# Performance work log

Hardware: AMD Instinct MI355X
Metric: run time of the kernel (lower is better)

The kernel has to match this reference:

```python
import jax, jax.numpy as jnp
import numpy as np
from jax import lax

BN_EPS = 1e-5
PAD = ((2, 3), (1, 2))  # 'same' padding for kernel (6,4): H pad 5 -> (2,3), W pad 3 -> (1,2)
DN = ('NCHW', 'OIHW', 'NCHW')


def _conv_block(x, w, b, g, bt, m, v, pool):
    # pool(bn(relu(conv(pad(x))))) as in the torch module (eval-mode BN)
    x = lax.conv_general_dilated(x, w, (1, 1), PAD, dimension_numbers=DN)
    x = jax.nn.relu(x + b[None, :, None, None])
    scale = g / jnp.sqrt(v + BN_EPS)
    x = (x - m[None, :, None, None]) * scale[None, :, None, None] + bt[None, :, None, None]
    win = (1, 1) + pool
    return lax.reduce_window(x, -jnp.inf, lax.max, win, win, 'VALID')


def _fc_bn(x, w, b, g, bt, m, v):
    x = jax.nn.relu(x @ w.T + b)
    return (x - m) * (g / jnp.sqrt(v + BN_EPS)) + bt


def _apply_cnn(x, p):
    x = x[:, None, :, :]  # [N,1,72,64]
    x = _conv_block(x, p['conv1_w'], p['conv1_b'], p['bnc1_g'], p['bnc1_b'], p['bnc1_m'], p['bnc1_v'], (2, 2))
    x = _conv_block(x, p['conv2_w'], p['conv2_b'], p['bnc2_g'], p['bnc2_b'], p['bnc2_m'], p['bnc2_v'], (2, 2))
    x = _conv_block(x, p['conv3_w'], p['conv3_b'], p['bnc3_g'], p['bnc3_b'], p['bnc3_m'], p['bnc3_v'], (3, 4))
    x = x.reshape(x.shape[0], 6 * 4 * 64)  # NCHW contiguous flatten matches torch .view
    x = _fc_bn(x, p['fc1_w'], p['fc1_b'], p['bnf1_g'], p['bnf1_b'], p['bnf1_m'], p['bnf1_v'])
    x = _fc_bn(x, p['fc2_w'], p['fc2_b'], p['bnf2_g'], p['bnf2_b'], p['bnf2_m'], p['bnf2_v'])
    x = _fc_bn(x, p['fc3_w'], p['fc3_b'], p['bnf3_g'], p['bnf3_b'], p['bnf3_m'], p['bnf3_v'])
    # F.normalize(x, p=2, dim=1) with eps=1e-12
    nrm = jnp.linalg.norm(x, axis=1, keepdims=True)
    return x / jnp.maximum(nrm, 1e-12)


def _ssm(embeds):
    # pairwise L2 distances via Gram trick (replaces the O(n^2) python loop)
    sq = jnp.sum(embeds * embeds, axis=1)  # [n]
    d2 = sq[:, None] + sq[None, :] - 2.0 * (embeds @ embeds.T)
    dist = jnp.sqrt(jnp.maximum(d2, 1e-12))
    dist = jnp.where(d2 > 0, dist, 0.0)  # exact zeros on diagonal, nan-safe grad
    return dist / jnp.max(dist)


def setup_inputs() -> dict:
    key = jax.random.key(0)
    ks = iter(jax.random.split(key, 64))
    d = {'x': jax.random.normal(next(ks), (512, 72, 64), jnp.float32)}

    def nrm(shape, s=0.05):
        return jax.random.normal(next(ks), shape, jnp.float32) * s

    def add_bn(name, c):
        d[name + '_g'] = 1.0 + nrm((c,))
        d[name + '_b'] = nrm((c,))
        d[name + '_m'] = nrm((c,), 0.1)
        d[name + '_v'] = 0.5 + jax.random.uniform(next(ks), (c,), jnp.float32)

    d['conv1_w'] = nrm((16, 1, 6, 4), 0.2);  d['conv1_b'] = nrm((16,));  add_bn('bnc1', 16)
    d['conv2_w'] = nrm((32, 16, 6, 4), 0.1); d['conv2_b'] = nrm((32,));  add_bn('bnc2', 32)
    d['conv3_w'] = nrm((64, 32, 6, 4), 0.05); d['conv3_b'] = nrm((64,)); add_bn('bnc3', 64)
    d['fc1_w'] = nrm((512, 1536), 0.03); d['fc1_b'] = nrm((512,)); add_bn('bnf1', 512)
    d['fc2_w'] = nrm((256, 512), 0.05);  d['fc2_b'] = nrm((256,)); add_bn('bnf2', 256)
    d['fc3_w'] = nrm((128, 256), 0.07);  d['fc3_b'] = nrm((128,)); add_bn('bnf3', 128)
    return d


def reference(x,
              conv1_w, conv1_b, bnc1_g, bnc1_b, bnc1_m, bnc1_v,
              conv2_w, conv2_b, bnc2_g, bnc2_b, bnc2_m, bnc2_v,
              conv3_w, conv3_b, bnc3_g, bnc3_b, bnc3_m, bnc3_v,
              fc1_w, fc1_b, bnf1_g, bnf1_b, bnf1_m, bnf1_v,
              fc2_w, fc2_b, bnf2_g, bnf2_b, bnf2_m, bnf2_v,
              fc3_w, fc3_b, bnf3_g, bnf3_b, bnf3_m, bnf3_v):
    p = dict(conv1_w=conv1_w, conv1_b=conv1_b, bnc1_g=bnc1_g, bnc1_b=bnc1_b, bnc1_m=bnc1_m, bnc1_v=bnc1_v,
             conv2_w=conv2_w, conv2_b=conv2_b, bnc2_g=bnc2_g, bnc2_b=bnc2_b, bnc2_m=bnc2_m, bnc2_v=bnc2_v,
             conv3_w=conv3_w, conv3_b=conv3_b, bnc3_g=bnc3_g, bnc3_b=bnc3_b, bnc3_m=bnc3_m, bnc3_v=bnc3_v,
             fc1_w=fc1_w, fc1_b=fc1_b, bnf1_g=bnf1_g, bnf1_b=bnf1_b, bnf1_m=bnf1_m, bnf1_v=bnf1_v,
             fc2_w=fc2_w, fc2_b=fc2_b, bnf2_g=bnf2_g, bnf2_b=bnf2_b, bnf2_m=bnf2_m, bnf2_v=bnf2_v,
             fc3_w=fc3_w, fc3_b=fc3_b, bnf3_g=bnf3_g, bnf3_b=bnf3_b, bnf3_m=bnf3_m, bnf3_v=bnf3_v)
    embeds = _apply_cnn(x, p)  # [n, 128], L2-normalized
    return _ssm(embeds)        # [n, n]
```

## Files before the change

kernel.cpp:

```cpp
#include <hip/hip_runtime.h>
#include <math.h>


#define BN_EPS 1e-5f

typedef __attribute__((ext_vector_type(8))) short short8;
typedef __attribute__((ext_vector_type(4))) float f32x4;

__device__ __forceinline__ unsigned short f2bf(float f) {
    unsigned u = __float_as_uint(f);
    u += 0x7fffu + ((u >> 16) & 1u);
    return (unsigned short)(u >> 16);
}

__global__ __launch_bounds__(256) void repack_k(
    const float* __restrict__ w1, const float* __restrict__ w2,
    const float* __restrict__ w3,
    const float* __restrict__ fw1, const float* __restrict__ fw2,
    const float* __restrict__ fw3,
    unsigned short* __restrict__ wT1b,
    unsigned short* __restrict__ wT2b, unsigned short* __restrict__ wT3b,
    unsigned short* __restrict__ fw1b, unsigned short* __restrict__ fw2b,
    unsigned short* __restrict__ fw3b, unsigned* __restrict__ mxslot)
{
    int t = blockIdx.x * 256 + threadIdx.x;
    if (t == 0) *mxslot = 0u;
    if (t < 512) {
        int k = t & 31, oc = t >> 5;
        wT1b[t] = (k < 24) ? f2bf(w1[oc * 24 + k]) : (unsigned short)0;
    }
    if (t < 12288) {
        int k = t & 31, oc = (t >> 5) & 31, kk = t >> 10;
        int ky = kk >> 1, kxp = kk & 1;
        int hi = k >> 4, ic = k & 15;
        int kx = 2 * kxp + hi;
        wT2b[t] = f2bf(w2[((oc * 16 + ic) * 6 + ky) * 4 + kx]);
    }
    if (t < 49152) {
        int ic = t & 31, oc = (t >> 5) & 63, kk = t >> 11;
        int ky = kk >> 2, kx = kk & 3;
        wT3b[t] = f2bf(w3[((oc * 32 + ic) * 6 + ky) * 4 + kx]);
    }
    if (t < 786432) fw1b[t] = f2bf(fw1[t]);
    if (t < 131072) fw2b[t] = f2bf(fw2[t]);
    if (t < 32768)  fw3b[t] = f2bf(fw3[t]);
}

__global__ __launch_bounds__(512) void conv_all(
    const float* __restrict__ x, const unsigned short* __restrict__ wT1,
    const unsigned short* __restrict__ wT2, const unsigned short* __restrict__ wT3,
    const float* __restrict__ c1b, const float* __restrict__ g1,
    const float* __restrict__ b1, const float* __restrict__ m1,
    const float* __restrict__ v1,
    const float* __restrict__ c2b, const float* __restrict__ g2,
    const float* __restrict__ b2, const float* __restrict__ m2,
    const float* __restrict__ v2,
    const float* __restrict__ c3b, const float* __restrict__ g3,
    const float* __restrict__ b3, const float* __restrict__ m3,
    const float* __restrict__ v3,
    unsigned short* __restrict__ out3)
{
    __shared__ __align__(16) unsigned short s_out1[41 * 36 * 16];
    __shared__ __align__(16) unsigned short s_un[24 * 20 * 32];
    const int tid = threadIdx.x, nl = blockIdx.x;
    const int lane = tid & 63, wave = tid >> 6;
    const int n = lane & 15, q = lane >> 4;
    unsigned short* pa = s_un;
    unsigned short* pb = s_un + 5372;

    {
        unsigned* z32 = (unsigned*)s_un;
        for (int i = tid; i < 5372; i += 512) z32[i] = 0u;
        uint4 z4; z4.x = z4.y = z4.z = z4.w = 0u;
        for (int pc = tid; pc < 324; pc += 512) {
            int row, colc;
            if (pc < 180) { row = pc / 36; colc = pc % 36; if (row >= 2) row += 36; }
            else { int pz = pc - 180; row = 2 + (pz >> 2); colc = (pz & 3) ? 32 + (pz & 3) : 0; }
            uint4* d = (uint4*)(s_out1 + ((size_t)row * 36 + colc) * 16);
            d[0] = z4; d[1] = z4;
        }
    }
    __syncthreads();
    {
        const float4* src = (const float4*)(x + (size_t)nl * 4608);
        for (int i = tid; i < 1152; i += 512) {
            float4 val = src[i];
            int f = i * 4, row = (f >> 6) + 2, c = (f & 63) + 1;
            unsigned short h0 = f2bf(val.x), h1 = f2bf(val.y);
            unsigned short h2 = f2bf(val.z), h3 = f2bf(val.w);
            unsigned short* ap = pa + row * 68 + c;
            ap[0] = h0; ap[1] = h1; ap[2] = h2; ap[3] = h3;
            unsigned* bp = (unsigned*)(pb + row * 68 + c + 1);
            bp[0] = (unsigned)h0 | ((unsigned)h1 << 16);
            bp[1] = (unsigned)h2 | ((unsigned)h3 << 16);
        }
    }
    const float sc1 = g1[n] * rsqrtf(v1[n] + BN_EPS);
    const float bb1 = c1b[n];
    const float mm1 = b1[n] - m1[n] * sc1;
    const short8 bfr1 = *(const short8*)(wT1 + n * 32 + q * 8);
    __syncthreads();

    for (int i = 0; i < 36; ++i) {
        int t = wave * 36 + i;
        int pooled = 4 * t + (n >> 2);
        int ph = pooled >> 5, pw = pooled & 31;
        int py = (n >> 1) & 1, px = n & 1;
        int oh = 2 * ph + py, ow = 2 * pw + px;
        int r0 = (oh + 2 * q) * 68;
        const unsigned* base = px ? (const unsigned*)(pb + r0 + ow + 1)
                                  : (const unsigned*)(pa + r0 + ow);
        uint4 uu;
        uu.x = base[0];  uu.y = base[1];
        uu.z = base[34]; uu.w = base[35];
        short8 afr = *reinterpret_cast<short8*>(&uu);
        f32x4 acc = (f32x4){0.f, 0.f, 0.f, 0.f};
        acc = __builtin_amdgcn_mfma_f32_16x16x32_bf16(afr, bfr1, acc, 0, 0, 0);
        int po = 4 * t + q, oph = po >> 5, opw = po & 31;
        float mx = fmaxf(fmaxf(acc[0], acc[1]), fmaxf(acc[2], acc[3]));
        float val = fmaxf(mx + bb1, 0.f) * sc1 + mm1;
        s_out1[((oph + 2) * 36 + (opw + 1)) * 16 + n] = f2bf(val);
    }
    __syncthreads();
    {
        uint4 z4; z4.x = z4.y = z4.z = z4.w = 0u;
        for (int pc = tid; pc < 192; pc += 512) {
            int row, colc;
            if (pc < 120) { row = pc / 20; colc = pc % 20; if (row >= 2) row += 18; }
            else { int pz = pc - 120; row = 2 + (pz >> 2); colc = (pz & 3) ? 16 + (pz & 3) : 0; }
            uint4* d = (uint4*)(s_un + ((size_t)row * 20 + colc) * 32);
            d[0] = z4; d[1] = z4; d[2] = z4; d[3] = z4;
        }
    }
    float bnb2[2], bns2[2], bnm2[2];
#pragma unroll
    for (int nt = 0; nt < 2; ++nt) {
        int oc = nt * 16 + n;
        float sc = g2[oc] * rsqrtf(v2[oc] + BN_EPS);
        bnb2[nt] = c2b[oc]; bns2[nt] = sc; bnm2[nt] = b2[oc] - m2[oc] * sc;
    }
    __syncthreads();

    for (int pp = wave; pp < 36; pp += 8) {
        int ph = pp >> 1, half = pp & 1;
        f32x4 acc[2][2];
#pragma unroll
        for (int ab = 0; ab < 2; ++ab)
#pragma unroll
            for (int nt = 0; nt < 2; ++nt) acc[ab][nt] = (f32x4){0.f, 0.f, 0.f, 0.f};
#pragma unroll
        for (int ky = 0; ky < 6; ++ky)
#pragma unroll
            for (int kxp = 0; kxp < 2; ++kxp) {
                int kk = ky * 2 + kxp;
                short8 w0 = *(const short8*)(wT2 + ((size_t)(kk * 32 + n) * 32) + q * 8);
                short8 w1 = *(const short8*)(wT2 + ((size_t)(kk * 32 + 16 + n) * 32) + q * 8);
                int col = half * 16 + n + 2 * kxp;
#pragma unroll
                for (int ab = 0; ab < 2; ++ab) {
                    int row = 2 * ph + ab + ky;
                    short8 afr = *(const short8*)(s_out1 + ((size_t)(row * 36 + col) * 16) + q * 8);
                    acc[ab][0] = __builtin_amdgcn_mfma_f32_16x16x32_bf16(afr, w0, acc[ab][0], 0, 0, 0);
                    acc[ab][1] = __builtin_amdgcn_mfma_f32_16x16x32_bf16(afr, w1, acc[ab][1], 0, 0, 0);
                }
            }
        int pw0 = half * 8 + q * 2;
#pragma unroll
        for (int nt = 0; nt < 2; ++nt) {
            int oc = nt * 16 + n;
            float p0 = fmaxf(fmaxf(acc[0][nt][0], acc[0][nt][1]),
                             fmaxf(acc[1][nt][0], acc[1][nt][1]));
            float p1 = fmaxf(fmaxf(acc[0][nt][2], acc[0][nt][3]),
                             fmaxf(acc[1][nt][2], acc[1][nt][3]));
            p0 = fmaxf(p0 + bnb2[nt], 0.f) * bns2[nt] + bnm2[nt];
            p1 = fmaxf(p1 + bnb2[nt], 0.f) * bns2[nt] + bnm2[nt];
            s_un[((size_t)(ph + 2) * 20 + (pw0 + 1)) * 32 + oc] = f2bf(p0);
            s_un[((size_t)(ph + 2) * 20 + (pw0 + 2)) * 32 + oc] = f2bf(p1);
        }
    }
    __syncthreads();

    for (int ch = wave; ch < 12; ch += 8) {
        int pr = ch >> 1, nth = ch & 1;
        f32x4 acc[3][2];
#pragma unroll
        for (int r = 0; r < 3; ++r)
#pragma unroll
            for (int t2 = 0; t2 < 2; ++t2) acc[r][t2] = (f32x4){0.f, 0.f, 0.f, 0.f};
#pragma unroll
        for (int ky = 0; ky < 6; ++ky)
#pragma unroll
            for (int kx = 0; kx < 4; ++kx) {
                int kk = ky * 4 + kx;
                short8 w0 = *(const short8*)(wT3 + ((size_t)(kk * 64 + nth * 32 + n) * 32) + q * 8);
                short8 w1 = *(const short8*)(wT3 + ((size_t)(kk * 64 + nth * 32 + 16 + n) * 32) + q * 8);
#pragma unroll
                for (int r = 0; r < 3; ++r) {
                    int row = 3 * pr + r + ky;
                    int col = n + kx;
                    short8 afr = *(const short8*)(s_un + ((size_t)(row * 20 + col) * 32) + q * 8);
                    acc[r][0] = __builtin_amdgcn_mfma_f32_16x16x32_bf16(afr, w0, acc[r][0], 0, 0, 0);
                    acc[r][1] = __builtin_amdgcn_mfma_f32_16x16x32_bf16(afr, w1, acc[r][1], 0, 0, 0);
                }
            }
        size_t ob = (size_t)nl * 1536;
#pragma unroll
        for (int t2 = 0; t2 < 2; ++t2) {
            int oc = nth * 32 + t2 * 16 + n;
            float sc = g3[oc] * rsqrtf(v3[oc] + BN_EPS);
            float mx = -3.4e38f;
#pragma unroll
            for (int r = 0; r < 3; ++r)
#pragma unroll
                for (int e = 0; e < 4; ++e) mx = fmaxf(mx, acc[r][t2][e]);
            float val = fmaxf(mx + c3b[oc], 0.f) * sc + (b3[oc] - m3[oc] * sc);
            out3[ob + (size_t)oc * 24 + pr * 4 + q] = f2bf(val);
        }
    }
}

__global__ __launch_bounds__(256) void fc_m(
    const unsigned short* __restrict__ A, const unsigned short* __restrict__ W,
    const float* __restrict__ bias, const float* __restrict__ g,
    const float* __restrict__ bt, const float* __restrict__ m,
    const float* __restrict__ v, unsigned short* __restrict__ out_b,
    float* __restrict__ out_f, int K, int N, int mode)
{
    const int tid = threadIdx.x;
    const int lane = tid & 63, wave = tid >> 6;
    const int n = lane & 15, q = lane >> 4;
    const int wr = wave >> 1, wc = wave & 1;
    const int r0 = blockIdx.y * 32 + wr * 16;
    const int c0 = blockIdx.x * 32 + wc * 16;
    const int col = c0 + n;

    float sc = g[col] * rsqrtf(v[col] + BN_EPS);
    float bb = bias[col];
    float mm = bt[col] - m[col] * sc;

    const unsigned short* Ap = A + (size_t)(r0 + n) * K + q * 8;
    const unsigned short* Bp = W + (size_t)col * K + q * 8;

    f32x4 acc = (f32x4){0.f, 0.f, 0.f, 0.f};
    for (int kk = 0; kk < K; kk += 64) {
        short8 a0 = *(const short8*)(Ap + kk);
        short8 b0 = *(const short8*)(Bp + kk);
        short8 a1 = *(const short8*)(Ap + kk + 32);
        short8 b1 = *(const short8*)(Bp + kk + 32);
        acc = __builtin_amdgcn_mfma_f32_16x16x32_bf16(a0, b0, acc, 0, 0, 0);
        acc = __builtin_amdgcn_mfma_f32_16x16x32_bf16(a1, b1, acc, 0, 0, 0);
    }
#pragma unroll
    for (int e = 0; e < 4; ++e) {
        int row = r0 + q * 4 + e;
        float val = fmaxf(acc[e] + bb, 0.f) * sc + mm;
        if (mode == 0) out_b[(size_t)row * N + col] = f2bf(val);
        else           out_f[(size_t)row * N + col] = val;
    }
}

__global__ __launch_bounds__(128) void norm_k(const float* __restrict__ f3,
                                              float* __restrict__ E,
                                              float* __restrict__ sq)
{
    __shared__ float red[2];
    const int row = blockIdx.x, tid = threadIdx.x;
    float vv = f3[row * 128 + tid];
    float s = vv * vv;
#pragma unroll
    for (int off = 32; off >= 1; off >>= 1) s += __shfl_down(s, off, 64);
    if ((tid & 63) == 0) red[tid >> 6] = s;
    __syncthreads();
    float total = red[0] + red[1];
    float nn = fmaxf(sqrtf(total), 1e-12f);
    E[row * 128 + tid] = vv / nn;
    if (tid == 0) sq[row] = total / (nn * nn);
}

__global__ __launch_bounds__(256) void dist_k(const float* __restrict__ E,
                                              const float* __restrict__ sq,
                                              float* __restrict__ D,
                                              unsigned* __restrict__ mxslot)
{
    __shared__ __align__(16) float Ei[16 * 132];
    __shared__ __align__(16) float Ej[16 * 132];
    __shared__ float red[256];
    const int tid = threadIdx.x;
    const int bi = blockIdx.y * 16, bj = blockIdx.x * 16;
    {
        int lr = tid >> 4, lc = (tid & 15) * 8;
        float4 a0 = *(const float4*)(E + (bi + lr) * 128 + lc);
        float4 a1 = *(const float4*)(E + (bi + lr) * 128 + lc + 4);
        *(float4*)(Ei + lr * 132 + lc) = a0;
        *(float4*)(Ei + lr * 132 + lc + 4) = a1;
        float4 b0 = *(const float4*)(E + (bj + lr) * 128 + lc);
        float4 b1 = *(const float4*)(E + (bj + lr) * 128 + lc + 4);
        *(float4*)(Ej + lr * 132 + lc) = b0;
        *(float4*)(Ej + lr * 132 + lc + 4) = b1;
    }
    __syncthreads();
    const int tx = tid & 15, ty = tid >> 4;
    float dot = 0.f;
#pragma unroll 4
    for (int k = 0; k < 128; k += 4) {
        float4 a = *(const float4*)(Ei + ty * 132 + k);
        float4 b = *(const float4*)(Ej + tx * 132 + k);
        dot = fmaf(a.x, b.x, dot); dot = fmaf(a.y, b.y, dot);
        dot = fmaf(a.z, b.z, dot); dot = fmaf(a.w, b.w, dot);
    }
    int i = bi + ty, j = bj + tx;
    float d2 = sq[i] + sq[j] - 2.f * dot;
    float dist = sqrtf(fmaxf(d2, 1e-12f));
    dist = (d2 > 0.f) ? dist : 0.f;
    if (i == j) dist = 0.f;
    D[i * 512 + j] = dist;
    red[tid] = dist;
    __syncthreads();
    for (int s2 = 128; s2 > 0; s2 >>= 1) {
        if (tid < s2) red[tid] = fmaxf(red[tid], red[tid + s2]);
        __syncthreads();
    }
    if (tid == 0) atomicMax(mxslot, __float_as_uint(red[0]));
}

__global__ __launch_bounds__(256) void scale_k(float* __restrict__ D,
                                               const unsigned* __restrict__ mxslot)
{
    int idx = blockIdx.x * 256 + threadIdx.x;
    float M = __uint_as_float(*mxslot);
    D[idx] = D[idx] / M;
}

extern "C" void kernel_launch(void* const* d_in, const int* in_sizes, int n_in,
                              void* d_out, int out_size, void* d_ws, size_t ws_size,
                              hipStream_t stream)
{
    (void)in_sizes; (void)n_in; (void)out_size; (void)ws_size;
    const float* x    = (const float*)d_in[0];
    const float* c1w  = (const float*)d_in[1];
    const float* c1b  = (const float*)d_in[2];
    const float* g1   = (const float*)d_in[3];
    const float* b1   = (const float*)d_in[4];
    const float* m1   = (const float*)d_in[5];
    const float* v1   = (const float*)d_in[6];
    const float* c2w  = (const float*)d_in[7];
    const float* c2b  = (const float*)d_in[8];
    const float* g2   = (const float*)d_in[9];
    const float* b2   = (const float*)d_in[10];
    const float* m2   = (const float*)d_in[11];
    const float* v2   = (const float*)d_in[12];
    const float* c3w  = (const float*)d_in[13];
    const float* c3b  = (const float*)d_in[14];
    const float* g3   = (const float*)d_in[15];
    const float* b3   = (const float*)d_in[16];
    const float* m3   = (const float*)d_in[17];
    const float* v3   = (const float*)d_in[18];
    const float* fw1  = (const float*)d_in[19];
    const float* fb1  = (const float*)d_in[20];
    const float* gf1  = (const float*)d_in[21];
    const float* bf1  = (const float*)d_in[22];
    const float* mf1  = (const float*)d_in[23];
    const float* vf1  = (const float*)d_in[24];
    const float* fw2  = (const float*)d_in[25];
    const float* fb2  = (const float*)d_in[26];
    const float* gf2  = (const float*)d_in[27];
    const float* bf2  = (const float*)d_in[28];
    const float* mf2  = (const float*)d_in[29];
    const float* vf2  = (const float*)d_in[30];
    const float* fw3  = (const float*)d_in[31];
    const float* fb3  = (const float*)d_in[32];
    const float* gf3  = (const float*)d_in[33];
    const float* bf3  = (const float*)d_in[34];
    const float* mf3  = (const float*)d_in[35];
    const float* vf3  = (const float*)d_in[36];

    float* ws = (float*)d_ws;
    float* E    = ws + 0;
    float* sq   = ws + 65536;
    float* f3v  = ws + 66048;
    unsigned* mx = (unsigned*)(ws + 131584);
    unsigned short* wT1b = (unsigned short*)(ws + 131600);
    unsigned short* wT2b = (unsigned short*)(ws + 131856);
    unsigned short* wT3b = (unsigned short*)(ws + 138000);
    unsigned short* fw1b = (unsigned short*)(ws + 162576);
    unsigned short* fw2b = (unsigned short*)(ws + 555792);
    unsigned short* fw3b = (unsigned short*)(ws + 621328);
    unsigned short* out3b= (unsigned short*)(ws + 637712);
    unsigned short* a1b  = (unsigned short*)(ws + 1030928);
    unsigned short* a2b  = (unsigned short*)(ws + 1162000);

    float* out = (float*)d_out;

    repack_k<<<3072, 256, 0, stream>>>(c1w, c2w, c3w, fw1, fw2, fw3,
                                       wT1b, wT2b, wT3b, fw1b, fw2b, fw3b, mx);
    conv_all<<<512, 512, 0, stream>>>(x, wT1b, wT2b, wT3b,
                                      c1b, g1, b1, m1, v1,
                                      c2b, g2, b2, m2, v2,
                                      c3b, g3, b3, m3, v3, out3b);
    fc_m<<<dim3(16, 16), 256, 0, stream>>>(out3b, fw1b, fb1, gf1, bf1, mf1, vf1,
                                           a1b, nullptr, 1536, 512, 0);
    fc_m<<<dim3(8, 16), 256, 0, stream>>>(a1b, fw2b, fb2, gf2, bf2, mf2, vf2,
                                          a2b, nullptr, 512, 256, 0);
    fc_m<<<dim3(4, 16), 256, 0, stream>>>(a2b, fw3b, fb3, gf3, bf3, mf3, vf3,
                                          nullptr, f3v, 256, 128, 1);
    norm_k<<<512, 128, 0, stream>>>(f3v, E, sq);
    dist_k<<<dim3(32, 32), 256, 0, stream>>>(E, sq, out, mx);
    scale_k<<<1024, 256, 0, stream>>>(out, mx);
}
```

Baseline: 218.6 us.

## Overlap FC weight conversion with conv, swizzle LDS, stage conv output, pipeline FC loads

Moves the FC weight fp32-to-bf16 conversion out of the repack kernel and into 464 extra blocks of the conv kernel, so it runs alongside the convolution work and uses vectorized float4 loads. It XOR-swizzles the shared-memory layouts of the stage-1 and stage-2 activations to reduce LDS bank conflicts, stages the conv3 output in LDS for a coalesced uint4 store, and software-pipelines the FC GEMM loop with two accumulators. Extra blocks add scheduling pressure to the conv kernel, and the swizzle adds index arithmetic.

```diff
diff --git a/kernel.cpp b/kernel.cpp
--- a/kernel.cpp
+++ b/kernel.cpp
@@ -16,12 +16,9 @@
 __global__ __launch_bounds__(256) void repack_k(
     const float* __restrict__ w1, const float* __restrict__ w2,
     const float* __restrict__ w3,
-    const float* __restrict__ fw1, const float* __restrict__ fw2,
-    const float* __restrict__ fw3,
     unsigned short* __restrict__ wT1b,
     unsigned short* __restrict__ wT2b, unsigned short* __restrict__ wT3b,
-    unsigned short* __restrict__ fw1b, unsigned short* __restrict__ fw2b,
-    unsigned short* __restrict__ fw3b, unsigned* __restrict__ mxslot)
+    unsigned* __restrict__ mxslot)
 {
     int t = blockIdx.x * 256 + threadIdx.x;
     if (t == 0) *mxslot = 0u;
@@ -41,9 +38,6 @@
         int ky = kk >> 2, kx = kk & 3;
         wT3b[t] = f2bf(w3[((oc * 32 + ic) * 6 + ky) * 4 + kx]);
     }
-    if (t < 786432) fw1b[t] = f2bf(fw1[t]);
-    if (t < 131072) fw2b[t] = f2bf(fw2[t]);
-    if (t < 32768)  fw3b[t] = f2bf(fw3[t]);
 }
 
 __global__ __launch_bounds__(512) void conv_all(
@@ -58,11 +52,29 @@
     const float* __restrict__ c3b, const float* __restrict__ g3,
     const float* __restrict__ b3, const float* __restrict__ m3,
     const float* __restrict__ v3,
+    const float* __restrict__ fw1, const float* __restrict__ fw2,
+    const float* __restrict__ fw3,
+    unsigned short* __restrict__ fw1b, unsigned short* __restrict__ fw2b,
+    unsigned short* __restrict__ fw3b,
     unsigned short* __restrict__ out3)
 {
     __shared__ __align__(16) unsigned short s_out1[41 * 36 * 16];
     __shared__ __align__(16) unsigned short s_un[24 * 20 * 32];
     const int tid = threadIdx.x, nl = blockIdx.x;
+
+    if (nl >= 512) {
+        int base = (nl - 512) * 2048 + tid * 4;
+        const float* src; unsigned short* dst; int off;
+        if (base < 786432)      { src = fw1; dst = fw1b; off = base; }
+        else if (base < 917504) { src = fw2; dst = fw2b; off = base - 786432; }
+        else                    { src = fw3; dst = fw3b; off = base - 917504; }
+        float4 v4 = *(const float4*)(src + off);
+        ushort4 o;
+        o.x = f2bf(v4.x); o.y = f2bf(v4.y); o.z = f2bf(v4.z); o.w = f2bf(v4.w);
+        *(ushort4*)(dst + off) = o;
+        return;
+    }
+
     const int lane = tid & 63, wave = tid >> 6;
     const int n = lane & 15, q = lane >> 4;
     unsigned short* pa = s_un;
@@ -119,7 +131,10 @@
         int po = 4 * t + q, oph = po >> 5, opw = po & 31;
         float mx = fmaxf(fmaxf(acc[0], acc[1]), fmaxf(acc[2], acc[3]));
         float val = fmaxf(mx + bb1, 0.f) * sc1 + mm1;
-        s_out1[((oph + 2) * 36 + (opw + 1)) * 16 + n] = f2bf(val);
+        int cc = (oph + 2) * 36 + (opw + 1);
+        int gsA = cc * 2 + (n >> 3);
+        gsA ^= (gsA >> 3) & 1;
+        s_out1[gsA * 8 + (n & 7)] = f2bf(val);
     }
     __syncthreads();
     {
@@ -159,7 +174,9 @@
 #pragma unroll
                 for (int ab = 0; ab < 2; ++ab) {
                     int row = 2 * ph + ab + ky;
-                    short8 afr = *(const short8*)(s_out1 + ((size_t)(row * 36 + col) * 16) + q * 8);
+                    int gsB = (row * 36 + col) * 2 + q;
+                    gsB ^= (gsB >> 3) & 1;
+                    short8 afr = *(const short8*)(s_out1 + gsB * 8);
                     acc[ab][0] = __builtin_amdgcn_mfma_f32_16x16x32_bf16(afr, w0, acc[ab][0], 0, 0, 0);
                     acc[ab][1] = __builtin_amdgcn_mfma_f32_16x16x32_bf16(afr, w1, acc[ab][1], 0, 0, 0);
                 }
@@ -174,12 +191,18 @@
                              fmaxf(acc[1][nt][2], acc[1][nt][3]));
             p0 = fmaxf(p0 + bnb2[nt], 0.f) * bns2[nt] + bnm2[nt];
             p1 = fmaxf(p1 + bnb2[nt], 0.f) * bns2[nt] + bnm2[nt];
-            s_un[((size_t)(ph + 2) * 20 + (pw0 + 1)) * 32 + oc] = f2bf(p0);
-            s_un[((size_t)(ph + 2) * 20 + (pw0 + 2)) * 32 + oc] = f2bf(p1);
+            int ca = pw0 + 1, cb = pw0 + 2;
+            int gA = ((ph + 2) * 20 + ca) * 4 + (oc >> 3);
+            gA ^= (gA >> 3) & 3;
+            s_un[gA * 8 + (oc & 7)] = f2bf(p0);
+            int gB = ((ph + 2) * 20 + cb) * 4 + (oc >> 3);
+            gB ^= (gB >> 3) & 3;
+            s_un[gB * 8 + (oc & 7)] = f2bf(p1);
         }
     }
     __syncthreads();
 
+    unsigned short* obuf = s_out1;
     for (int ch = wave; ch < 12; ch += 8) {
         int pr = ch >> 1, nth = ch & 1;
         f32x4 acc[3][2];
@@ -194,16 +217,17 @@
                 int kk = ky * 4 + kx;
                 short8 w0 = *(const short8*)(wT3 + ((size_t)(kk * 64 + nth * 32 + n) * 32) + q * 8);
                 short8 w1 = *(const short8*)(wT3 + ((size_t)(kk * 64 + nth * 32 + 16 + n) * 32) + q * 8);
+                int col = n + kx;
 #pragma unroll
                 for (int r = 0; r < 3; ++r) {
                     int row = 3 * pr + r + ky;
-                    int col = n + kx;
-                    short8 afr = *(const short8*)(s_un + ((size_t)(row * 20 + col) * 32) + q * 8);
+                    int gC = (row * 20 + col) * 4 + q;
+                    gC ^= (gC >> 3) & 3;
+                    short8 afr = *(const short8*)(s_un + gC * 8);
                     acc[r][0] = __builtin_amdgcn_mfma_f32_16x16x32_bf16(afr, w0, acc[r][0], 0, 0, 0);
                     acc[r][1] = __builtin_amdgcn_mfma_f32_16x16x32_bf16(afr, w1, acc[r][1], 0, 0, 0);
                 }
             }
-        size_t ob = (size_t)nl * 1536;
 #pragma unroll
         for (int t2 = 0; t2 < 2; ++t2) {
             int oc = nth * 32 + t2 * 16 + n;
@@ -214,8 +238,14 @@
 #pragma unroll
                 for (int e = 0; e < 4; ++e) mx = fmaxf(mx, acc[r][t2][e]);
             float val = fmaxf(mx + c3b[oc], 0.f) * sc + (b3[oc] - m3[oc] * sc);
-            out3[ob + (size_t)oc * 24 + pr * 4 + q] = f2bf(val);
+            obuf[oc * 24 + pr * 4 + q] = f2bf(val);
         }
+    }
+    __syncthreads();
+    {
+        const uint4* srcv = (const uint4*)obuf;
+        uint4* dstv = (uint4*)(out3 + (size_t)nl * 1536);
+        for (int i = tid; i < 192; i += 512) dstv[i] = srcv[i];
     }
 }
 
@@ -241,19 +271,28 @@
     const unsigned short* Ap = A + (size_t)(r0 + n) * K + q * 8;
     const unsigned short* Bp = W + (size_t)col * K + q * 8;
 
-    f32x4 acc = (f32x4){0.f, 0.f, 0.f, 0.f};
-    for (int kk = 0; kk < K; kk += 64) {
-        short8 a0 = *(const short8*)(Ap + kk);
-        short8 b0 = *(const short8*)(Bp + kk);
-        short8 a1 = *(const short8*)(Ap + kk + 32);
-        short8 b1 = *(const short8*)(Bp + kk + 32);
-        acc = __builtin_amdgcn_mfma_f32_16x16x32_bf16(a0, b0, acc, 0, 0, 0);
-        acc = __builtin_amdgcn_mfma_f32_16x16x32_bf16(a1, b1, acc, 0, 0, 0);
-    }
+    f32x4 acc0 = (f32x4){0.f, 0.f, 0.f, 0.f};
+    f32x4 acc1 = (f32x4){0.f, 0.f, 0.f, 0.f};
+    short8 a0 = *(const short8*)(Ap);
+    short8 b0 = *(const short8*)(Bp);
+    short8 a1 = *(const short8*)(Ap + 32);
+    short8 b1 = *(const short8*)(Bp + 32);
+#pragma unroll 2
+    for (int kk = 64; kk < K; kk += 64) {
+        short8 a0n = *(const short8*)(Ap + kk);
+        short8 b0n = *(const short8*)(Bp + kk);
+        short8 a1n = *(const short8*)(Ap + kk + 32);
+        short8 b1n = *(const short8*)(Bp + kk + 32);
+        acc0 = __builtin_amdgcn_mfma_f32_16x16x32_bf16(a0, b0, acc0, 0, 0, 0);
+        acc1 = __builtin_amdgcn_mfma_f32_16x16x32_bf16(a1, b1, acc1, 0, 0, 0);
+        a0 = a0n; b0 = b0n; a1 = a1n; b1 = b1n;
+    }
+    acc0 = __builtin_amdgcn_mfma_f32_16x16x32_bf16(a0, b0, acc0, 0, 0, 0);
+    acc1 = __builtin_amdgcn_mfma_f32_16x16x32_bf16(a1, b1, acc1, 0, 0, 0);
 #pragma unroll
     for (int e = 0; e < 4; ++e) {
         int row = r0 + q * 4 + e;
-        float val = fmaxf(acc[e] + bb, 0.f) * sc + mm;
+        float val = fmaxf(acc0[e] + acc1[e] + bb, 0.f) * sc + mm;
         if (mode == 0) out_b[(size_t)row * N + col] = f2bf(val);
         else           out_f[(size_t)row * N + col] = val;
     }
@@ -391,12 +430,12 @@
 
     float* out = (float*)d_out;
 
-    repack_k<<<3072, 256, 0, stream>>>(c1w, c2w, c3w, fw1, fw2, fw3,
-                                       wT1b, wT2b, wT3b, fw1b, fw2b, fw3b, mx);
-    conv_all<<<512, 512, 0, stream>>>(x, wT1b, wT2b, wT3b,
+    repack_k<<<192, 256, 0, stream>>>(c1w, c2w, c3w, wT1b, wT2b, wT3b, mx);
+    conv_all<<<976, 512, 0, stream>>>(x, wT1b, wT2b, wT3b,
                                       c1b, g1, b1, m1, v1,
                                       c2b, g2, b2, m2, v2,
-                                      c3b, g3, b3, m3, v3, out3b);
+                                      c3b, g3, b3, m3, v3,
+                                      fw1, fw2, fw3, fw1b, fw2b, fw3b, out3b);
     fc_m<<<dim3(16, 16), 256, 0, stream>>>(out3b, fw1b, fb1, gf1, bf1, mf1, vf1,
                                            a1b, nullptr, 1536, 512, 0);
     fc_m<<<dim3(8, 16), 256, 0, stream>>>(a1b, fw2b, fb2, gf2, bf2, mf2, vf2,
```

Result: slower. 226.7 us (+3.7%).
